# Kernel optimization log

Measured on AMD Instinct MI355X. Metric: run time of the kernel, lower is better.

## Reference

```python
import jax, jax.numpy as jnp
import numpy as np

L, D, H, HD = 2, 2048, 16, 128          # layers, hidden, heads, head_dim
E, K, F, FS = 8, 2, 1408, 5632           # experts, top_k, moe_inter, shared_inter
V, T = 32000, 2048                       # vocab, tokens
EPS = 1e-6
ROPE_BASE = 1000000.0


def _rms(x, w):
    return x * jax.lax.rsqrt(jnp.mean(x * x, axis=-1, keepdims=True) + EPS) * w


def _rope(x, cos, sin):
    half = x.shape[-1] // 2
    x1, x2 = x[..., :half], x[..., half:]
    return jnp.concatenate([x1 * cos - x2 * sin, x1 * sin + x2 * cos], axis=-1)


def setup_inputs() -> dict:
    key = jax.random.key(0)
    ks = jax.random.split(key, 18)
    s = 0.02
    f = lambda k, shp: jax.random.normal(k, shp, jnp.float32) * s
    return {
        "input_ids": jax.random.randint(ks[0], (T,), 0, V, dtype=jnp.int32),
        "positions": jnp.arange(T, dtype=jnp.int32),
        "embed": f(ks[1], (V, D)),
        "qw": f(ks[2], (L, D, H * HD)),
        "kw": f(ks[3], (L, D, H * HD)),
        "vw": f(ks[4], (L, D, H * HD)),
        "ow": f(ks[5], (L, H * HD, D)),
        "ln1": jnp.ones((L, D), jnp.float32),
        "ln2": jnp.ones((L, D), jnp.float32),
        "router_w": f(ks[6], (L, D, E)),
        "sgate_w": f(ks[7], (L, D)),
        "wg": f(ks[8], (L, E, D, F)),
        "wu": f(ks[9], (L, E, D, F)),
        "wd": f(ks[10], (L, E, F, D)),
        "swg": f(ks[11], (L, D, FS)),
        "swu": f(ks[12], (L, D, FS)),
        "swd": f(ks[13], (L, FS, D)),
        "final_ln": jnp.ones((D,), jnp.float32),
    }


def _attn(x, positions, qw_l, kw_l, vw_l, ow_l):
    q = (x @ qw_l).reshape(T, H, HD)
    k = (x @ kw_l).reshape(T, H, HD)
    v = (x @ vw_l).reshape(T, H, HD)
    half = HD // 2
    inv = 1.0 / (ROPE_BASE ** (jnp.arange(half, dtype=jnp.float32) / half))
    ang = positions.astype(jnp.float32)[:, None] * inv[None, :]  # [T, half]
    cos, sin = jnp.cos(ang)[:, None, :], jnp.sin(ang)[:, None, :]
    q = _rope(q, cos, sin)
    k = _rope(k, cos, sin)
    scores = jnp.einsum('thd,shd->hts', q, k) * (HD ** -0.5)  # [H, T, T]
    mask = positions[:, None] >= positions[None, :]  # causal
    scores = jnp.where(mask[None], scores, -1e30)
    p = jax.nn.softmax(scores, axis=-1)
    o = jnp.einsum('hts,shd->thd', p, v).reshape(T, H * HD)
    return o @ ow_l


def _moe(x, router_w_l, sgate_w_l, wg_l, wu_l, wd_l, swg_l, swu_l, swd_l):
    # shared expert + its sigmoid gate
    sh = (jax.nn.silu(x @ swg_l) * (x @ swu_l)) @ swd_l
    sgate = jax.nn.sigmoid(x @ sgate_w_l)[:, None]
    # router: softmax in float32, then top-k with prob renorm (norm_topk_prob)
    probs = jax.nn.softmax((x @ router_w_l).astype(jnp.float32), axis=-1)
    topv, topi = jax.lax.top_k(probs, K)
    topv = topv / jnp.sum(topv, axis=-1, keepdims=True)
    combine = jnp.sum(jax.nn.one_hot(topi, E, dtype=x.dtype) * topv[..., None].astype(x.dtype), axis=1)  # [T, E]
    # dense grouped expert FFN, combined by routing weights (scatter-add equivalent)
    g = jnp.einsum('td,edf->etf', x, wg_l)
    u = jnp.einsum('td,edf->etf', x, wu_l)
    y = jnp.einsum('etf,efd->etd', jax.nn.silu(g) * u, wd_l)
    moe_out = jnp.einsum('te,etd->td', combine, y)
    return (moe_out + sgate * sh) * (1.0 / K ** 0.5)


def reference(input_ids, positions, embed, qw, kw, vw, ow, ln1, ln2, router_w,
              sgate_w, wg, wu, wd, swg, swu, swd, final_ln):
    h = embed[input_ids]  # [T, D]
    residual = None
    for l in range(L):
        if residual is None:
            residual = h
            x = _rms(h, ln1[l])
        else:
            residual = h + residual
            x = _rms(residual, ln1[l])
        h = _attn(x, positions, qw[l], kw[l], vw[l], ow[l])
        residual = h + residual
        x = _rms(residual, ln2[l])
        h = _moe(x, router_w[l], sgate_w[l], wg[l], wu[l], wd[l], swg[l], swu[l], swd[l])
    residual = h + residual
    return _rms(residual, final_ln)
```

## Files before the change

### kernel.cpp

```cpp
#include <hip/hip_runtime.h>
#include <stdint.h>

#define TT 2048
#define DD 2048
#define HH 16
#define HDIM 128
#define NE 8
#define TOPK 2
#define FF 1408
#define FSS 5632
#define NL 2

typedef __bf16 bf16;
typedef __bf16 bf16x2 __attribute__((ext_vector_type(2)));
typedef __bf16 bf16x4 __attribute__((ext_vector_type(4)));
typedef __bf16 bf16x8 __attribute__((ext_vector_type(8)));
typedef float f32x4 __attribute__((ext_vector_type(4)));

__device__ __forceinline__ void split1(float f, bf16& h, bf16& l) {
  bf16 hb = (bf16)f;
  h = hb;
  l = (bf16)(f - (float)hb);
}

__device__ __forceinline__ void gload16(const void* g, void* l) {
  __builtin_amdgcn_global_load_lds((const __attribute__((address_space(1))) void*)g,
                                   (__attribute__((address_space(3))) void*)l, 16, 0, 0);
}

template<bool LO>
__launch_bounds__(256)
__global__ void k_wtrans(const float* __restrict__ W, bf16* __restrict__ Wh,
                         bf16* __restrict__ Wl, int Kd, int N, int nofs, int Ntot)
{
  __shared__ float T[64][68];
  const size_t slabIn  = (size_t)blockIdx.z * (size_t)Kd * (size_t)N;
  const size_t slabOut = (size_t)blockIdx.z * (size_t)Kd * (size_t)Ntot;
  const float* Wp = W + slabIn;
  const int k0 = blockIdx.x * 64, n0 = blockIdx.y * 64;
  const int tid = threadIdx.x;
  const int rr = tid >> 2, c4 = (tid & 3) * 4;
  const float* src = Wp + (size_t)(k0 + rr) * N + n0 + c4;
#pragma unroll
  for (int j = 0; j < 4; ++j) {
    f32x4 v = *(const f32x4*)(src + j * 16);
    *(f32x4*)&T[rr][c4 + j * 16] = v;
  }
  __syncthreads();
  const int nn = tid >> 2, kk = (tid & 3) * 16;
  bf16x8 h0, h1, l0, l1;
#pragma unroll
  for (int j = 0; j < 8; ++j) {
    bf16 hb, lb;
    split1(T[kk + j][nn], hb, lb);
    h0[j] = hb; l0[j] = lb;
    split1(T[kk + 8 + j][nn], hb, lb);
    h1[j] = hb; l1[j] = lb;
  }
  size_t out = slabOut + (size_t)(nofs + n0 + nn) * Kd + k0 + kk;
  *(bf16x8*)&Wh[out] = h0;
  *(bf16x8*)&Wh[out + 8] = h1;
  if (LO) {
    *(bf16x8*)&Wl[out] = l0;
    *(bf16x8*)&Wl[out + 8] = l1;
  }
}

template<int BMT, int NT, bool EXPERT, bool GATHER, int OM>
__launch_bounds__(256, (BMT == 128 ? 3 : 4))
__global__ void k_gemmp(const bf16* __restrict__ Ah, const bf16* __restrict__ Al,
                        const bf16* __restrict__ Bh, const bf16* __restrict__ Bl,
                        void* __restrict__ C1, void* __restrict__ C2,
                        void* __restrict__ C3, void* __restrict__ C4,
                        void* __restrict__ C5, void* __restrict__ C6,
                        int M, int N, int Kd, int lda, int ldc,
                        const int* __restrict__ perm, const int* __restrict__ cnt,
                        const int* __restrict__ ofs)
{
  constexpr int PL = (NT == 3) ? 2 : 1;
  constexpr int ASUB = BMT / 16;
  constexpr int AISS = PL * ASUB;
  constexpr int BISS = PL * 8;
  constexpr int QPW = (AISS + BISS) / 4;
  constexpr int IF = BMT / 32;

  const int bx = EXPERT ? (int)blockIdx.x
               : ((int)blockIdx.x & 7) * ((int)gridDim.x >> 3) + ((int)blockIdx.x >> 3);

  int m_count = M, row_base = 0;
  size_t boff = 0;
  if (EXPERT) {
    int e = blockIdx.z;
    m_count = cnt[e];
    if (bx * BMT >= m_count) return;
    row_base = ofs[e];
    boff = (size_t)e * (size_t)N * (size_t)Kd;
  }
  const int tid = threadIdx.x, lane = tid & 63, wid = tid >> 6;
  const int wm = (wid >> 1) * (BMT / 2), wn = (wid & 1) * 64;
  const int lr = lane & 15, g = lane >> 4;
  const int n0 = blockIdx.y * 128;
  const int m0 = bx * BMT;

  __shared__ bf16 As[PL][BMT][32];
  __shared__ bf16 Bs[PL][128][32];

  const bf16* srcp[QPW];
#pragma unroll
  for (int j = 0; j < QPW; ++j) {
    int q = wid * QPW + j;
    int r16 = lane >> 2;
    int kc = (lane & 3) ^ ((lane >> 3) & 3);
    if (q < AISS) {
      int pl = q / ASUB, sub = q % ASUB;
      int r = sub * 16 + r16;
      int tok;
      if (EXPERT) {
        int lrow = m0 + r;
        if (lrow >= m_count) lrow = m_count - 1;
        tok = GATHER ? perm[row_base + lrow] : (row_base + lrow);
      } else {
        tok = m0 + r;
      }
      const bf16* base = (pl == 0) ? Ah : Al;
      srcp[j] = base + (size_t)tok * lda + kc * 8;
    } else {
      int qb = q - AISS;
      int pl = qb >> 3, sub = qb & 7;
      int nrow = sub * 16 + r16;
      const bf16* base = (pl == 0) ? Bh : Bl;
      srcp[j] = base + boff + (size_t)(n0 + nrow) * Kd + kc * 8;
    }
  }

  f32x4 acc[IF][4];
#pragma unroll
  for (int i = 0; i < IF; ++i)
#pragma unroll
    for (int j = 0; j < 4; ++j)
      acc[i][j] = (f32x4){0.f, 0.f, 0.f, 0.f};

  auto ISSUE = [&](int k0) {
#pragma unroll
    for (int j = 0; j < QPW; ++j) {
      int q = wid * QPW + j;
      bf16* dst;
      if (q < AISS) {
        int pl = q / ASUB, sub = q % ASUB;
        dst = &As[pl][sub * 16][0];
      } else {
        int qb = q - AISS;
        int pl = qb >> 3, sub = qb & 7;
        dst = &Bs[pl][sub * 16][0];
      }
      gload16(srcp[j] + k0, dst);
    }
  };

  const int gs = (g ^ ((lr >> 1) & 3)) * 8;
  const int NTk = Kd >> 5;
  ISSUE(0);
  for (int t = 0; t < NTk; ++t) {
    __syncthreads();
    bf16x8 bfr[4][PL], afr[IF][PL];
#pragma unroll
    for (int jj = 0; jj < 4; ++jj)
#pragma unroll
      for (int pl = 0; pl < PL; ++pl)
        bfr[jj][pl] = *(const bf16x8*)&Bs[pl][wn + jj * 16 + lr][gs];
#pragma unroll
    for (int i = 0; i < IF; ++i)
#pragma unroll
      for (int pl = 0; pl < PL; ++pl)
        afr[i][pl] = *(const bf16x8*)&As[pl][wm + i * 16 + lr][gs];
    __syncthreads();
    if (t + 1 < NTk) ISSUE((t + 1) << 5);
#pragma unroll
    for (int i = 0; i < IF; ++i)
#pragma unroll
      for (int jj = 0; jj < 4; ++jj) {
        f32x4 a2 = acc[i][jj];
        a2 = __builtin_amdgcn_mfma_f32_16x16x32_bf16(afr[i][0], bfr[jj][0], a2, 0, 0, 0);
        if (NT == 3) {
          a2 = __builtin_amdgcn_mfma_f32_16x16x32_bf16(afr[i][0], bfr[jj][1], a2, 0, 0, 0);
          a2 = __builtin_amdgcn_mfma_f32_16x16x32_bf16(afr[i][1], bfr[jj][0], a2, 0, 0, 0);
        }
        acc[i][jj] = a2;
      }
  }

  void *O1 = C1, *O2 = C2;
  bool otrans = (OM == 4);
  int coff = 0;
  if (OM == 5) {
    int seg = n0 / ldc;
    coff = seg * ldc;
    if (seg == 1)      { O1 = C3; O2 = C4; }
    else if (seg == 2) { O1 = C5; O2 = C6; otrans = true; }
  } else if (OM == 6) {
    int seg = n0 / ldc;
    coff = seg * ldc;
    if (seg) O1 = C3;
  }

  const int r0 = g * 4;
#pragma unroll
  for (int i = 0; i < IF; ++i) {
    int lrow0 = m0 + wm + i * 16 + r0;
#pragma unroll
    for (int j = 0; j < 4; ++j) {
      int col = n0 + wn + j * 16 + lr - coff;
      if (OM == 4 || (OM == 5 && otrans)) {
        bf16x4 ph, pl;
#pragma unroll
        for (int r = 0; r < 4; ++r) { bf16 hb, lb; split1(acc[i][j][r], hb, lb); ph[r] = hb; pl[r] = lb; }
        *(bf16x4*)&((bf16*)O1)[(size_t)col * ldc + lrow0] = ph;
        *(bf16x4*)&((bf16*)O2)[(size_t)col * ldc + lrow0] = pl;
      } else {
#pragma unroll
        for (int r = 0; r < 4; ++r) {
          int lrow = lrow0 + r;
          if (EXPERT && lrow >= m_count) continue;
          size_t off = (size_t)(row_base + lrow) * ldc + col;
          if (OM == 1 || OM == 6) {
            ((float*)O1)[off] = acc[i][j][r];
          } else {
            bf16 hb, lb; split1(acc[i][j][r], hb, lb);
            ((bf16*)O1)[off] = hb;
            ((bf16*)O2)[off] = lb;
          }
        }
      }
    }
  }
}

__launch_bounds__(256)
__global__ void k_attns(const bf16* __restrict__ Qh, const bf16* __restrict__ Ql,
                        const bf16* __restrict__ Kh, const bf16* __restrict__ Kl,
                        const bf16* __restrict__ Vh, const bf16* __restrict__ Vl,
                        bf16* __restrict__ Oh, bf16* __restrict__ Ol)
{
  const int tid = threadIdx.x;
  const int lane = tid & 63, wid = tid >> 6;
  const int head = blockIdx.y;
  const int qbase = (gridDim.x - 1 - blockIdx.x) * 32;
  const int lr = lane & 15, g = lane >> 4;

  __shared__ float o_l[4][16][132];
  __shared__ float m_l[4][16], l_l[4][16];
  bf16* plbase = (bf16*)&o_l[0][0][0];
  bf16 (*pl_h)[40] = (bf16(*)[40])(plbase + wid * 16 * 40);
  bf16 (*pl_l)[40] = (bf16(*)[40])(plbase + (4 + wid) * 16 * 40);

  bf16x8 qfhA[4], qflA[4], qfhB[4], qflB[4];
  {
    size_t qoffA = (size_t)(qbase + lr) * DD + head * HDIM;
    size_t qoffB = qoffA + (size_t)16 * DD;
#pragma unroll
    for (int c = 0; c < 4; ++c) {
      qfhA[c] = *(const bf16x8*)(Qh + qoffA + c * 32 + g * 8);
      qflA[c] = *(const bf16x8*)(Ql + qoffA + c * 32 + g * 8);
      qfhB[c] = *(const bf16x8*)(Qh + qoffB + c * 32 + g * 8);
      qflB[c] = *(const bf16x8*)(Ql + qoffB + c * 32 + g * 8);
    }
  }

  f32x4 oA[8], oB[8];
#pragma unroll
  for (int d = 0; d < 8; ++d) {
    oA[d] = (f32x4){0.f, 0.f, 0.f, 0.f};
    oB[d] = (f32x4){0.f, 0.f, 0.f, 0.f};
  }
  float mA = -1e30f, lA = 0.f;
  float mB = -1e30f, lB = 0.f;

  const int qend = qbase + 32;
  for (int kb = wid * 32; kb < qend; kb += 128) {
    f32x4 sA0 = {0.f,0.f,0.f,0.f}, sA1 = {0.f,0.f,0.f,0.f};
    f32x4 sB0 = {0.f,0.f,0.f,0.f}, sB1 = {0.f,0.f,0.f,0.f};
    size_t k0off = (size_t)(kb + lr) * DD + head * HDIM;
    size_t k1off = k0off + (size_t)16 * DD;
#pragma unroll
    for (int c = 0; c < 4; ++c) {
      bf16x8 kh0 = *(const bf16x8*)(Kh + k0off + c * 32 + g * 8);
      bf16x8 kl0 = *(const bf16x8*)(Kl + k0off + c * 32 + g * 8);
      sA0 = __builtin_amdgcn_mfma_f32_16x16x32_bf16(kh0, qfhA[c], sA0, 0, 0, 0);
      sA0 = __builtin_amdgcn_mfma_f32_16x16x32_bf16(kl0, qfhA[c], sA0, 0, 0, 0);
      sA0 = __builtin_amdgcn_mfma_f32_16x16x32_bf16(kh0, qflA[c], sA0, 0, 0, 0);
      sB0 = __builtin_amdgcn_mfma_f32_16x16x32_bf16(kh0, qfhB[c], sB0, 0, 0, 0);
      sB0 = __builtin_amdgcn_mfma_f32_16x16x32_bf16(kl0, qfhB[c], sB0, 0, 0, 0);
      sB0 = __builtin_amdgcn_mfma_f32_16x16x32_bf16(kh0, qflB[c], sB0, 0, 0, 0);
      bf16x8 kh1 = *(const bf16x8*)(Kh + k1off + c * 32 + g * 8);
      bf16x8 kl1 = *(const bf16x8*)(Kl + k1off + c * 32 + g * 8);
      sA1 = __builtin_amdgcn_mfma_f32_16x16x32_bf16(kh1, qfhA[c], sA1, 0, 0, 0);
      sA1 = __builtin_amdgcn_mfma_f32_16x16x32_bf16(kl1, qfhA[c], sA1, 0, 0, 0);
      sA1 = __builtin_amdgcn_mfma_f32_16x16x32_bf16(kh1, qflA[c], sA1, 0, 0, 0);
      sB1 = __builtin_amdgcn_mfma_f32_16x16x32_bf16(kh1, qfhB[c], sB1, 0, 0, 0);
      sB1 = __builtin_amdgcn_mfma_f32_16x16x32_bf16(kl1, qfhB[c], sB1, 0, 0, 0);
      sB1 = __builtin_amdgcn_mfma_f32_16x16x32_bf16(kh1, qflB[c], sB1, 0, 0, 0);
    }
    float p0A[4], p1A[4];
    {
      float mloc = -1e30f;
      const int q = qbase + lr;
#pragma unroll
      for (int r = 0; r < 4; ++r) {
        int k0i = kb + g * 4 + r;
        float a0 = sA0[r] * 0.08838834764831845f;
        float a1 = sA1[r] * 0.08838834764831845f;
        if (k0i > q)      a0 = -1e30f;
        if (k0i + 16 > q) a1 = -1e30f;
        p0A[r] = a0; p1A[r] = a1;
        mloc = fmaxf(mloc, fmaxf(a0, a1));
      }
      mloc = fmaxf(mloc, __shfl_xor(mloc, 16, 64));
      mloc = fmaxf(mloc, __shfl_xor(mloc, 32, 64));
      float mn = fmaxf(mA, mloc);
      float alpha = __expf(mA - mn);
      mA = mn;
      float ps = 0.f;
#pragma unroll
      for (int r = 0; r < 4; ++r) {
        p0A[r] = __expf(p0A[r] - mn);
        p1A[r] = __expf(p1A[r] - mn);
        ps += p0A[r] + p1A[r];
      }
      ps += __shfl_xor(ps, 16, 64);
      ps += __shfl_xor(ps, 32, 64);
      lA = lA * alpha + ps;
      float alr[4];
#pragma unroll
      for (int r = 0; r < 4; ++r) alr[r] = __shfl(alpha, g * 4 + r, 64);
#pragma unroll
      for (int d = 0; d < 8; ++d)
#pragma unroll
        for (int r = 0; r < 4; ++r) oA[d][r] *= alr[r];
    }
    float p0B[4], p1B[4];
    {
      float mloc = -1e30f;
      const int q = qbase + 16 + lr;
#pragma unroll
      for (int r = 0; r < 4; ++r) {
        int k0i = kb + g * 4 + r;
        float a0 = sB0[r] * 0.08838834764831845f;
        float a1 = sB1[r] * 0.08838834764831845f;
        if (k0i > q)      a0 = -1e30f;
        if (k0i + 16 > q) a1 = -1e30f;
        p0B[r] = a0; p1B[r] = a1;
        mloc = fmaxf(mloc, fmaxf(a0, a1));
      }
      mloc = fmaxf(mloc, __shfl_xor(mloc, 16, 64));
      mloc = fmaxf(mloc, __shfl_xor(mloc, 32, 64));
      float mn = fmaxf(mB, mloc);
      float alpha = __expf(mB - mn);
      mB = mn;
      float ps = 0.f;
#pragma unroll
      for (int r = 0; r < 4; ++r) {
        p0B[r] = __expf(p0B[r] - mn);
        p1B[r] = __expf(p1B[r] - mn);
        ps += p0B[r] + p1B[r];
      }
      ps += __shfl_xor(ps, 16, 64);
      ps += __shfl_xor(ps, 32, 64);
      lB = lB * alpha + ps;
      float alr[4];
#pragma unroll
      for (int r = 0; r < 4; ++r) alr[r] = __shfl(alpha, g * 4 + r, 64);
#pragma unroll
      for (int d = 0; d < 8; ++d)
#pragma unroll
        for (int r = 0; r < 4; ++r) oB[d][r] *= alr[r];
    }
#pragma unroll
    for (int r = 0; r < 4; ++r) {
      bf16 hb, lb;
      split1(p0A[r], hb, lb);
      pl_h[lr][g * 4 + r] = hb;
      pl_l[lr][g * 4 + r] = lb;
      split1(p1A[r], hb, lb);
      pl_h[lr][16 + g * 4 + r] = hb;
      pl_l[lr][16 + g * 4 + r] = lb;
    }
    bf16x8 pahA = *(const bf16x8*)&pl_h[lr][g * 8];
    bf16x8 palA = *(const bf16x8*)&pl_l[lr][g * 8];
#pragma unroll
    for (int r = 0; r < 4; ++r) {
      bf16 hb, lb;
      split1(p0B[r], hb, lb);
      pl_h[lr][g * 4 + r] = hb;
      pl_l[lr][g * 4 + r] = lb;
      split1(p1B[r], hb, lb);
      pl_h[lr][16 + g * 4 + r] = hb;
      pl_l[lr][16 + g * 4 + r] = lb;
    }
    bf16x8 pahB = *(const bf16x8*)&pl_h[lr][g * 8];
    bf16x8 palB = *(const bf16x8*)&pl_l[lr][g * 8];
#pragma unroll
    for (int d = 0; d < 8; ++d) {
      size_t voff = (size_t)(head * HDIM + d * 16 + lr) * TT + kb + g * 8;
      bf16x8 vfh = *(const bf16x8*)(Vh + voff);
      bf16x8 vfl = *(const bf16x8*)(Vl + voff);
      oA[d] = __builtin_amdgcn_mfma_f32_16x16x32_bf16(pahA, vfh, oA[d], 0, 0, 0);
      oA[d] = __builtin_amdgcn_mfma_f32_16x16x32_bf16(pahA, vfl, oA[d], 0, 0, 0);
      oA[d] = __builtin_amdgcn_mfma_f32_16x16x32_bf16(palA, vfh, oA[d], 0, 0, 0);
      oB[d] = __builtin_amdgcn_mfma_f32_16x16x32_bf16(pahB, vfh, oB[d], 0, 0, 0);
      oB[d] = __builtin_amdgcn_mfma_f32_16x16x32_bf16(pahB, vfl, oB[d], 0, 0, 0);
      oB[d] = __builtin_amdgcn_mfma_f32_16x16x32_bf16(palB, vfh, oB[d], 0, 0, 0);
    }
  }

  __syncthreads();
  if (g == 0) {
    m_l[wid][lr] = mA;
    l_l[wid][lr] = lA;
  }
#pragma unroll
  for (int d = 0; d < 8; ++d)
#pragma unroll
    for (int r = 0; r < 4; ++r)
      o_l[wid][g * 4 + r][d * 16 + lr] = oA[d][r];
  __syncthreads();
  {
    const int row = tid >> 4;
    const int c0 = (tid & 15) * 8;
    float m0v = m_l[0][row], m1v = m_l[1][row], m2v = m_l[2][row], m3v = m_l[3][row];
    float ms = fmaxf(fmaxf(m0v, m1v), fmaxf(m2v, m3v));
    float s0v = __expf(m0v - ms), s1v = __expf(m1v - ms);
    float s2v = __expf(m2v - ms), s3v = __expf(m3v - ms);
    float lsum = l_l[0][row] * s0v + l_l[1][row] * s1v
               + l_l[2][row] * s2v + l_l[3][row] * s3v;
    float inv = 1.f / lsum;
    union { bf16 b[8]; uint4 u; } ph, pl;
#pragma unroll
    for (int j = 0; j < 8; ++j) {
      float v = o_l[0][row][c0 + j] * s0v + o_l[1][row][c0 + j] * s1v
              + o_l[2][row][c0 + j] * s2v + o_l[3][row][c0 + j] * s3v;
      bf16 hb, lb;
      split1(v * inv, hb, lb);
      ph.b[j] = hb; pl.b[j] = lb;
    }
    size_t oi = (size_t)(qbase + row) * DD + head * HDIM + c0;
    *(uint4*)(Oh + oi) = ph.u;
    *(uint4*)(Ol + oi) = pl.u;
  }
  __syncthreads();
  if (g == 0) {
    m_l[wid][lr] = mB;
    l_l[wid][lr] = lB;
  }
#pragma unroll
  for (int d = 0; d < 8; ++d)
#pragma unroll
    for (int r = 0; r < 4; ++r)
      o_l[wid][g * 4 + r][d * 16 + lr] = oB[d][r];
  __syncthreads();
  {
    const int row = tid >> 4;
    const int c0 = (tid & 15) * 8;
    float m0v = m_l[0][row], m1v = m_l[1][row], m2v = m_l[2][row], m3v = m_l[3][row];
    float ms = fmaxf(fmaxf(m0v, m1v), fmaxf(m2v, m3v));
    float s0v = __expf(m0v - ms), s1v = __expf(m1v - ms);
    float s2v = __expf(m2v - ms), s3v = __expf(m3v - ms);
    float lsum = l_l[0][row] * s0v + l_l[1][row] * s1v
               + l_l[2][row] * s2v + l_l[3][row] * s3v;
    float inv = 1.f / lsum;
    union { bf16 b[8]; uint4 u; } ph, pl;
#pragma unroll
    for (int j = 0; j < 8; ++j) {
      float v = o_l[0][row][c0 + j] * s0v + o_l[1][row][c0 + j] * s1v
              + o_l[2][row][c0 + j] * s2v + o_l[3][row][c0 + j] * s3v;
      bf16 hb, lb;
      split1(v * inv, hb, lb);
      ph.b[j] = hb; pl.b[j] = lb;
    }
    size_t oi = (size_t)(qbase + 16 + row) * DD + head * HDIM + c0;
    *(uint4*)(Oh + oi) = ph.u;
    *(uint4*)(Ol + oi) = pl.u;
  }
}

__global__ void k_embed(const int* __restrict__ ids, const float* __restrict__ Em,
                        float* __restrict__ Hout)
{
  int t = blockIdx.x, tid = threadIdx.x;
  const float4* s = (const float4*)(Em + (size_t)ids[t] * DD);
  float4* dst = (float4*)(Hout + (size_t)t * DD);
  dst[tid] = s[tid];
  dst[tid + 256] = s[tid + 256];
}

template<bool ADDIN, bool WF32, bool FINAL>
__launch_bounds__(256)
__global__ void k_addrms(const float* __restrict__ Hin, float* __restrict__ Res,
                         const float* __restrict__ W,
                         bf16* __restrict__ Xh, bf16* __restrict__ Xl,
                         float* __restrict__ Xf)
{
  const int t = blockIdx.x, tid = threadIdx.x;
  const size_t base = (size_t)t * DD + tid * 8;
  float x[8];
  {
    const float4* hp = (const float4*)(Hin + base);
    float4 a = hp[0], b = hp[1];
    x[0]=a.x; x[1]=a.y; x[2]=a.z; x[3]=a.w;
    x[4]=b.x; x[5]=b.y; x[6]=b.z; x[7]=b.w;
    if (ADDIN) {
      const float4* rp = (const float4*)(Res + base);
      float4 c = rp[0], d = rp[1];
      x[0]+=c.x; x[1]+=c.y; x[2]+=c.z; x[3]+=c.w;
      x[4]+=d.x; x[5]+=d.y; x[6]+=d.z; x[7]+=d.w;
    }
  }
  {
    float4* rp = (float4*)(Res + base);
    rp[0] = make_float4(x[0], x[1], x[2], x[3]);
    rp[1] = make_float4(x[4], x[5], x[6], x[7]);
  }
  float ss = 0.f;
#pragma unroll
  for (int j = 0; j < 8; ++j) ss += x[j] * x[j];
#pragma unroll
  for (int off = 32; off; off >>= 1) ss += __shfl_xor(ss, off, 64);
  __shared__ float red[4];
  if ((tid & 63) == 0) red[tid >> 6] = ss;
  __syncthreads();
  float tot = red[0] + red[1] + red[2] + red[3];
  float sc = rsqrtf(tot * (1.0f / DD) + 1e-6f);
  float y[8];
#pragma unroll
  for (int j = 0; j < 8; ++j) y[j] = x[j] * sc * W[tid * 8 + j];
  if (!FINAL) {
    union { bf16 b[8]; uint4 u; } ph, pl;
#pragma unroll
    for (int j = 0; j < 8; ++j) { bf16 hb, lb; split1(y[j], hb, lb); ph.b[j] = hb; pl.b[j] = lb; }
    *(uint4*)(Xh + base) = ph.u;
    *(uint4*)(Xl + base) = pl.u;
  }
  if (WF32 || FINAL) {
    float4* xp = (float4*)(Xf + base);
    xp[0] = make_float4(y[0], y[1], y[2], y[3]);
    xp[1] = make_float4(y[4], y[5], y[6], y[7]);
  }
}

__global__ void k_rope2(bf16* __restrict__ Qh, bf16* __restrict__ Ql,
                        bf16* __restrict__ Kh, bf16* __restrict__ Kl,
                        const int* __restrict__ pos)
{
  int idx = blockIdx.x * 256 + threadIdx.x;
  int d = idx & 63;
  int h = (idx >> 6) & (HH - 1);
  int t = idx >> 10;
  if (t >= TT) return;
  double inv = pow(1.0e6, -(double)d / 64.0);
  double ang = (double)pos[t] * inv;
  double sd, cd;
  sincos(ang, &sd, &cd);
  float sn = (float)sd, cs = (float)cd;
  size_t base = (size_t)t * DD + h * HDIM + d;
  float q1 = (float)Qh[base] + (float)Ql[base];
  float q2 = (float)Qh[base + 64] + (float)Ql[base + 64];
  float qa = q1 * cs - q2 * sn, qb = q1 * sn + q2 * cs;
  bf16 hb, lb;
  split1(qa, hb, lb); Qh[base] = hb;      Ql[base] = lb;
  split1(qb, hb, lb); Qh[base + 64] = hb; Ql[base + 64] = lb;
  float k1 = (float)Kh[base] + (float)Kl[base];
  float k2 = (float)Kh[base + 64] + (float)Kl[base + 64];
  float ka = k1 * cs - k2 * sn, kb2 = k1 * sn + k2 * cs;
  split1(ka, hb, lb);  Kh[base] = hb;      Kl[base] = lb;
  split1(kb2, hb, lb); Kh[base + 64] = hb; Kl[base + 64] = lb;
}

__launch_bounds__(64)
__global__ void k_router(const float* __restrict__ Xf, const float* __restrict__ RW,
                         const float* __restrict__ SGW, int* __restrict__ eidx,
                         float* __restrict__ ew, float* __restrict__ sgate,
                         int* __restrict__ cnt)
{
  const int t = blockIdx.x, lane = threadIdx.x;
  const float* x = Xf + (size_t)t * DD;
  float acc[8] = {0,0,0,0,0,0,0,0};
  float sg = 0.f;
  for (int i = lane; i < DD; i += 64) {
    float xv = x[i];
    const float4* w = (const float4*)(RW + (size_t)i * NE);
    float4 w0 = w[0], w1 = w[1];
    acc[0] += xv * w0.x; acc[1] += xv * w0.y; acc[2] += xv * w0.z; acc[3] += xv * w0.w;
    acc[4] += xv * w1.x; acc[5] += xv * w1.y; acc[6] += xv * w1.z; acc[7] += xv * w1.w;
    sg += xv * SGW[i];
  }
#pragma unroll
  for (int off = 32; off; off >>= 1) {
#pragma unroll
    for (int e = 0; e < 8; ++e) acc[e] += __shfl_xor(acc[e], off, 64);
    sg += __shfl_xor(sg, off, 64);
  }
  if (lane == 0) {
    int i0 = 0; float v0 = acc[0];
    for (int e = 1; e < 8; ++e) if (acc[e] > v0) { v0 = acc[e]; i0 = e; }
    int i1 = -1; float v1 = -1e30f;
    for (int e = 0; e < 8; ++e) if (e != i0 && acc[e] > v1) { v1 = acc[e]; i1 = e; }
    float w0 = 1.f / (1.f + expf(v1 - v0));
    eidx[2*t] = i0; eidx[2*t+1] = i1;
    ew[2*t] = w0; ew[2*t+1] = 1.f - w0;
    sgate[t] = 1.f / (1.f + expf(-sg));
    atomicAdd(&cnt[i0], 1);
    atomicAdd(&cnt[i1], 1);
  }
}

__global__ void k_scan(const int* __restrict__ cnt, int* __restrict__ ofs)
{
  if (threadIdx.x == 0) {
    int s = 0;
    for (int e = 0; e < NE; ++e) { ofs[e] = s; s += cnt[e]; }
    ofs[NE] = s;
  }
}

__global__ void k_assign(const int* __restrict__ eidx, const int* __restrict__ ofs,
                         int* __restrict__ cursor, int* __restrict__ perm,
                         int* __restrict__ posof)
{
  int t = blockIdx.x * 256 + threadIdx.x;
  if (t >= TT) return;
#pragma unroll
  for (int j = 0; j < 2; ++j) {
    int e = eidx[2*t + j];
    int p = ofs[e] + atomicAdd(&cursor[e], 1);
    perm[p] = t;
    posof[2*t + j] = p;
  }
}

__global__ void k_silup(const float* __restrict__ G, const float* __restrict__ U,
                        bf16* __restrict__ H, bf16* __restrict__ L)
{
  int i = (blockIdx.x * 256 + threadIdx.x) * 4;
  float4 g = *(const float4*)(G + i);
  float4 u = *(const float4*)(U + i);
  float s[4];
  s[0] = g.x / (1.f + expf(-g.x)) * u.x;
  s[1] = g.y / (1.f + expf(-g.y)) * u.y;
  s[2] = g.z / (1.f + expf(-g.z)) * u.z;
  s[3] = g.w / (1.f + expf(-g.w)) * u.w;
  bf16x4 h, l;
#pragma unroll
  for (int j = 0; j < 4; ++j) { bf16 hb, lb; split1(s[j], hb, lb); h[j] = hb; l[j] = lb; }
  *(bf16x4*)(H + i) = h;
  *(bf16x4*)(L + i) = l;
}

__global__ void k_combine(const float* __restrict__ Y, const float* __restrict__ SH,
                          const float* __restrict__ sgate, const float* __restrict__ ew,
                          const int* __restrict__ posof, float* __restrict__ Hout)
{
  int t = blockIdx.x, tid = threadIdx.x;
  int p0 = posof[2*t], p1 = posof[2*t+1];
  float w0 = ew[2*t], w1 = ew[2*t+1];
  float sgv = sgate[t];
  int d0 = tid * 8;
  const float4* a = (const float4*)(Y + (size_t)p0 * DD + d0);
  const float4* b = (const float4*)(Y + (size_t)p1 * DD + d0);
  float4 a0 = a[0], a1 = a[1], b0 = b[0], b1 = b[1];
  float y0[8] = {a0.x,a0.y,a0.z,a0.w,a1.x,a1.y,a1.z,a1.w};
  float y1[8] = {b0.x,b0.y,b0.z,b0.w,b1.x,b1.y,b1.z,b1.w};
  const float4* shp = (const float4*)(SH + (size_t)t * DD + d0);
  float4 sa = shp[0], sb = shp[1];
  float shv[8] = {sa.x, sa.y, sa.z, sa.w, sb.x, sb.y, sb.z, sb.w};
  float out[8];
#pragma unroll
  for (int j = 0; j < 8; ++j)
    out[j] = (y0[j] * w0 + y1[j] * w1 + sgv * shv[j]) * 0.70710678118654752f;
  float4* op = (float4*)(Hout + (size_t)t * DD + d0);
  op[0] = make_float4(out[0], out[1], out[2], out[3]);
  op[1] = make_float4(out[4], out[5], out[6], out[7]);
}

extern "C" void kernel_launch(void* const* d_in, const int* in_sizes, int n_in,
                              void* d_out, int out_size, void* d_ws, size_t ws_size,
                              hipStream_t stream)
{
  (void)in_sizes; (void)n_in; (void)out_size; (void)ws_size;
  const int*   ids  = (const int*)d_in[0];
  const int*   pos  = (const int*)d_in[1];
  const float* emb  = (const float*)d_in[2];
  const float* qw   = (const float*)d_in[3];
  const float* kw   = (const float*)d_in[4];
  const float* vw   = (const float*)d_in[5];
  const float* ow   = (const float*)d_in[6];
  const float* ln1  = (const float*)d_in[7];
  const float* ln2  = (const float*)d_in[8];
  const float* rw   = (const float*)d_in[9];
  const float* sgw  = (const float*)d_in[10];
  const float* wg   = (const float*)d_in[11];
  const float* wu   = (const float*)d_in[12];
  const float* wd   = (const float*)d_in[13];
  const float* swg  = (const float*)d_in[14];
  const float* swu  = (const float*)d_in[15];
  const float* swd  = (const float*)d_in[16];
  const float* fln  = (const float*)d_in[17];

  char* p = (char*)d_ws;
  auto alloc = [&](size_t b) { char* r = p; p += (b + 255) & ~(size_t)255; return r; };

  const size_t TD = (size_t)TT * DD;
  float* resid = (float*)alloc(TD * 4);
  float* hbuf  = (float*)alloc(TD * 4);
  float* xf    = (float*)alloc(TD * 4);
  bf16*  xh    = (bf16*) alloc(TD * 2);
  bf16*  xl    = (bf16*) alloc(TD * 2);
  bf16*  qhb   = (bf16*) alloc(TD * 2);
  bf16*  qlb   = (bf16*) alloc(TD * 2);
  bf16*  khb   = (bf16*) alloc(TD * 2);
  bf16*  klb   = (bf16*) alloc(TD * 2);
  bf16*  vth   = (bf16*) alloc(TD * 2);
  bf16*  vtl   = (bf16*) alloc(TD * 2);
  bf16*  aoh   = (bf16*) alloc(TD * 2);
  bf16*  aol   = (bf16*) alloc(TD * 2);
  float* shb   = (float*)alloc(TD * 4);
  const size_t SGF = (size_t)TT * FSS;
  const size_t GEF = (size_t)TT * TOPK * FF;
  bf16*  shph  = (bf16*) alloc(SGF * 2);
  bf16*  shpl  = (bf16*) alloc(SGF * 2);
  bf16*  geph  = (bf16*) alloc(GEF * 2);
  bf16*  gepl  = (bf16*) alloc(GEF * 2);
  float* region = (float*)alloc(2 * SGF * 4);
  float* sgbf = region;
  float* subf = region + SGF;
  float* gebf = region;
  float* uebf = region + GEF;
  float* ybf  = region + 2 * GEF;
  const size_t WME = (size_t)NE * DD * FF;
  bf16* wbh = (bf16*)alloc(WME * 2);
  bf16* wbl = (bf16*)alloc(WME * 2);
  int*   eidx  = (int*)  alloc((size_t)TT * TOPK * 4);
  float* ewb   = (float*)alloc((size_t)TT * TOPK * 4);
  float* sgate = (float*)alloc((size_t)TT * 4);
  int*   perm  = (int*)  alloc((size_t)TT * TOPK * 4);
  int*   posof = (int*)  alloc((size_t)TT * TOPK * 4);
  int*   cnt   = (int*)  alloc(64);
  int*   ofs   = (int*)  alloc(64);
  int*   cursor = cnt + 8;

  k_embed<<<TT, 256, 0, stream>>>(ids, emb, hbuf);

  for (int l = 0; l < NL; ++l) {
    const float* qw_l  = qw  + (size_t)l * DD * DD;
    const float* kw_l  = kw  + (size_t)l * DD * DD;
    const float* vw_l  = vw  + (size_t)l * DD * DD;
    const float* ow_l  = ow  + (size_t)l * DD * DD;
    const float* ln1_l = ln1 + (size_t)l * DD;
    const float* ln2_l = ln2 + (size_t)l * DD;
    const float* rw_l  = rw  + (size_t)l * DD * NE;
    const float* sgw_l = sgw + (size_t)l * DD;
    const float* wg_l  = wg  + (size_t)l * NE * DD * FF;
    const float* wu_l  = wu  + (size_t)l * NE * DD * FF;
    const float* wd_l  = wd  + (size_t)l * NE * FF * DD;
    const float* swg_l = swg + (size_t)l * DD * FSS;
    const float* swu_l = swu + (size_t)l * DD * FSS;
    const float* swd_l = swd + (size_t)l * FSS * DD;
    const bool last = (l == NL - 1);

    if (l == 0)
      k_addrms<false,false,false><<<TT,256,0,stream>>>(hbuf, resid, ln1_l, xh, xl, nullptr);
    else
      k_addrms<true, false,false><<<TT,256,0,stream>>>(hbuf, resid, ln1_l, xh, xl, nullptr);

    k_wtrans<true><<<dim3(32,32),256,0,stream>>>(qw_l, wbh, wbl, DD, DD, 0,    3*DD);
    k_wtrans<true><<<dim3(32,32),256,0,stream>>>(kw_l, wbh, wbl, DD, DD, DD,   3*DD);
    k_wtrans<true><<<dim3(32,32),256,0,stream>>>(vw_l, wbh, wbl, DD, DD, 2*DD, 3*DD);
    k_gemmp<64,3,false,false,5><<<dim3(32,48),256,0,stream>>>(xh, xl, wbh, wbl,
        qhb, qlb, khb, klb, vth, vtl, TT, 3*DD, DD, DD, DD, nullptr,nullptr,nullptr);
    k_rope2<<<(TT*HH*64)/256, 256, 0, stream>>>(qhb, qlb, khb, klb, pos);
    k_attns<<<dim3(TT/32, HH), 256, 0, stream>>>(qhb, qlb, khb, klb, vth, vtl, aoh, aol);
    k_wtrans<true><<<dim3(32,32),256,0,stream>>>(ow_l, wbh, wbl, DD, DD, 0, DD);
    k_gemmp<64,3,false,false,1><<<dim3(32,16),256,0,stream>>>(aoh, aol, wbh, wbl,
        hbuf, nullptr, nullptr, nullptr, nullptr, nullptr, TT, DD, DD, DD, DD, nullptr,nullptr,nullptr);

    k_addrms<true,true,false><<<TT,256,0,stream>>>(hbuf, resid, ln2_l, xh, xl, xf);

    hipMemsetAsync(cnt, 0, 64, stream);
    k_router<<<TT, 64, 0, stream>>>(xf, rw_l, sgw_l, eidx, ewb, sgate, cnt);
    k_scan<<<1, 64, 0, stream>>>(cnt, ofs);
    k_assign<<<TT/256, 256, 0, stream>>>(eidx, ofs, cursor, perm, posof);

    if (!last) {
      k_wtrans<true><<<dim3(32,88),256,0,stream>>>(swg_l, wbh, wbl, DD, FSS, 0,   2*FSS);
      k_wtrans<true><<<dim3(32,88),256,0,stream>>>(swu_l, wbh, wbl, DD, FSS, FSS, 2*FSS);
      k_gemmp<128,3,false,false,6><<<dim3(16,88),256,0,stream>>>(xh, xl, wbh, wbl,
          sgbf, nullptr, subf, nullptr, nullptr, nullptr, TT, 2*FSS, DD, DD, FSS, nullptr,nullptr,nullptr);
      k_silup<<<(TT*FSS/4)/256, 256, 0, stream>>>(sgbf, subf, shph, shpl);
      k_wtrans<true><<<dim3(88,32),256,0,stream>>>(swd_l, wbh, wbl, FSS, DD, 0, DD);
      k_gemmp<64,3,false,false,1><<<dim3(32,16),256,0,stream>>>(shph, shpl, wbh, wbl,
          shb, nullptr, nullptr, nullptr, nullptr, nullptr, TT, DD, FSS, FSS, DD, nullptr,nullptr,nullptr);
    } else {
      k_wtrans<false><<<dim3(32,88),256,0,stream>>>(swg_l, wbh, wbl, DD, FSS, 0,   2*FSS);
      k_wtrans<false><<<dim3(32,88),256,0,stream>>>(swu_l, wbh, wbl, DD, FSS, FSS, 2*FSS);
      k_gemmp<128,1,false,false,6><<<dim3(16,88),256,0,stream>>>(xh, xl, wbh, wbl,
          sgbf, nullptr, subf, nullptr, nullptr, nullptr, TT, 2*FSS, DD, DD, FSS, nullptr,nullptr,nullptr);
      k_silup<<<(TT*FSS/4)/256, 256, 0, stream>>>(sgbf, subf, shph, shpl);
      k_wtrans<false><<<dim3(88,32),256,0,stream>>>(swd_l, wbh, wbl, FSS, DD, 0, DD);
      k_gemmp<64,1,false,false,1><<<dim3(32,16),256,0,stream>>>(shph, shpl, wbh, wbl,
          shb, nullptr, nullptr, nullptr, nullptr, nullptr, TT, DD, FSS, FSS, DD, nullptr,nullptr,nullptr);
    }

    if (!last) {
      k_wtrans<true><<<dim3(32,22,NE),256,0,stream>>>(wg_l, wbh, wbl, DD, FF, 0, FF);
      k_gemmp<64,3,true,true,1><<<dim3(64,11,NE),256,0,stream>>>(xh, xl, wbh, wbl,
          gebf, nullptr, nullptr, nullptr, nullptr, nullptr, TT, FF, DD, DD, FF, perm, cnt, ofs);
      k_wtrans<true><<<dim3(32,22,NE),256,0,stream>>>(wu_l, wbh, wbl, DD, FF, 0, FF);
      k_gemmp<64,3,true,true,1><<<dim3(64,11,NE),256,0,stream>>>(xh, xl, wbh, wbl,
          uebf, nullptr, nullptr, nullptr, nullptr, nullptr, TT, FF, DD, DD, FF, perm, cnt, ofs);
      k_silup<<<(GEF/4)/256, 256, 0, stream>>>(gebf, uebf, geph, gepl);
      k_wtrans<true><<<dim3(22,32,NE),256,0,stream>>>(wd_l, wbh, wbl, FF, DD, 0, DD);
      k_gemmp<64,3,true,false,1><<<dim3(64,16,NE),256,0,stream>>>(geph, gepl, wbh, wbl,
          ybf, nullptr, nullptr, nullptr, nullptr, nullptr, TT, DD, FF, FF, DD, nullptr, cnt, ofs);
    } else {
      k_wtrans<false><<<dim3(32,22,NE),256,0,stream>>>(wg_l, wbh, wbl, DD, FF, 0, FF);
      k_gemmp<64,1,true,true,1><<<dim3(64,11,NE),256,0,stream>>>(xh, xl, wbh, wbl,
          gebf, nullptr, nullptr, nullptr, nullptr, nullptr, TT, FF, DD, DD, FF, perm, cnt, ofs);
      k_wtrans<false><<<dim3(32,22,NE),256,0,stream>>>(wu_l, wbh, wbl, DD, FF, 0, FF);
      k_gemmp<64,1,true,true,1><<<dim3(64,11,NE),256,0,stream>>>(xh, xl, wbh, wbl,
          uebf, nullptr, nullptr, nullptr, nullptr, nullptr, TT, FF, DD, DD, FF, perm, cnt, ofs);
      k_silup<<<(GEF/4)/256, 256, 0, stream>>>(gebf, uebf, geph, gepl);
      k_wtrans<false><<<dim3(22,32,NE),256,0,stream>>>(wd_l, wbh, wbl, FF, DD, 0, DD);
      k_gemmp<64,1,true,false,1><<<dim3(64,16,NE),256,0,stream>>>(geph, gepl, wbh, wbl,
          ybf, nullptr, nullptr, nullptr, nullptr, nullptr, TT, DD, FF, FF, DD, nullptr, cnt, ofs);
    }
    k_combine<<<TT, 256, 0, stream>>>(ybf, shb, sgate, ewb, posof, hbuf);
  }

  k_addrms<true,false,true><<<TT,256,0,stream>>>(hbuf, resid, fln, nullptr, nullptr, (float*)d_out);
}
```

Measured before the change: 3.621 ms.

## Double-buffer GEMM shared-memory tiles with explicit vmcnt-based prefetch two steps ahead

Turns the single-buffered LDS tiles in the main GEMM kernel into two buffers and prefetches the K-tile two steps ahead. Each step waits only on the older load group through explicit s_waitcnt vmcnt and raw barriers, so global-to-LDS traffic overlaps the MFMA work. This doubles the shared-memory footprint, so the launch-bounds occupancy targets for the three-pass split-precision variants are lowered to make room. The hand-written waitcnt counts assume each thread issues exactly QPW loads per stage, which is a correctness risk.

```diff
diff --git a/kernel.cpp b/kernel.cpp
--- a/kernel.cpp
+++ b/kernel.cpp
@@ -67,7 +67,7 @@
 }
 
 template<int BMT, int NT, bool EXPERT, bool GATHER, int OM>
-__launch_bounds__(256, (BMT == 128 ? 3 : 4))
+__launch_bounds__(256, (NT == 3 ? (BMT == 128 ? 2 : 3) : 4))
 __global__ void k_gemmp(const bf16* __restrict__ Ah, const bf16* __restrict__ Al,
                         const bf16* __restrict__ Bh, const bf16* __restrict__ Bl,
                         void* __restrict__ C1, void* __restrict__ C2,
@@ -102,8 +102,8 @@
   const int n0 = blockIdx.y * 128;
   const int m0 = bx * BMT;
 
-  __shared__ bf16 As[PL][BMT][32];
-  __shared__ bf16 Bs[PL][128][32];
+  __shared__ bf16 As[2][PL][BMT][32];
+  __shared__ bf16 Bs[2][PL][128][32];
 
   const bf16* srcp[QPW];
 #pragma unroll
@@ -140,18 +140,18 @@
     for (int j = 0; j < 4; ++j)
       acc[i][j] = (f32x4){0.f, 0.f, 0.f, 0.f};
 
-  auto ISSUE = [&](int k0) {
+  auto ISSUE = [&](int buf, int k0) {
 #pragma unroll
     for (int j = 0; j < QPW; ++j) {
       int q = wid * QPW + j;
       bf16* dst;
       if (q < AISS) {
         int pl = q / ASUB, sub = q % ASUB;
-        dst = &As[pl][sub * 16][0];
+        dst = &As[buf][pl][sub * 16][0];
       } else {
         int qb = q - AISS;
         int pl = qb >> 3, sub = qb & 7;
-        dst = &Bs[pl][sub * 16][0];
+        dst = &Bs[buf][pl][sub * 16][0];
       }
       gload16(srcp[j] + k0, dst);
     }
@@ -159,22 +159,34 @@
 
   const int gs = (g ^ ((lr >> 1) & 3)) * 8;
   const int NTk = Kd >> 5;
-  ISSUE(0);
+  ISSUE(0, 0);
+  ISSUE(1, 32);
   for (int t = 0; t < NTk; ++t) {
-    __syncthreads();
+    const int cb = t & 1;
+    if (t + 1 < NTk) {
+      asm volatile("s_waitcnt vmcnt(%0)" :: "n"(QPW) : "memory");
+    } else {
+      asm volatile("s_waitcnt vmcnt(0)" ::: "memory");
+    }
+    __builtin_amdgcn_sched_barrier(0);
+    __builtin_amdgcn_s_barrier();
+    __builtin_amdgcn_sched_barrier(0);
     bf16x8 bfr[4][PL], afr[IF][PL];
 #pragma unroll
     for (int jj = 0; jj < 4; ++jj)
 #pragma unroll
       for (int pl = 0; pl < PL; ++pl)
-        bfr[jj][pl] = *(const bf16x8*)&Bs[pl][wn + jj * 16 + lr][gs];
+        bfr[jj][pl] = *(const bf16x8*)&Bs[cb][pl][wn + jj * 16 + lr][gs];
 #pragma unroll
     for (int i = 0; i < IF; ++i)
 #pragma unroll
       for (int pl = 0; pl < PL; ++pl)
-        afr[i][pl] = *(const bf16x8*)&As[pl][wm + i * 16 + lr][gs];
-    __syncthreads();
-    if (t + 1 < NTk) ISSUE((t + 1) << 5);
+        afr[i][pl] = *(const bf16x8*)&As[cb][pl][wm + i * 16 + lr][gs];
+    asm volatile("s_waitcnt lgkmcnt(0)" ::: "memory");
+    __builtin_amdgcn_sched_barrier(0);
+    __builtin_amdgcn_s_barrier();
+    __builtin_amdgcn_sched_barrier(0);
+    if (t + 2 < NTk) ISSUE(cb, (t + 2) << 5);
 #pragma unroll
     for (int i = 0; i < IF; ++i)
 #pragma unroll
```

New measurement: 3.672 ms. No clear change (+1.4%).
